# Optimization experiments

Measured on AMD Instinct MI355X. Metric: run time of the kernel, lower is better.

The kernel has to match this reference:

```python
import jax, jax.numpy as jnp
import numpy as np

NC = 20
IMG = 416
SCALES = (13, 26, 52)
B = 64
N = 32


def setup_inputs() -> dict:
    key = jax.random.key(0)
    k1, k2, k3, k4, k5, k6 = jax.random.split(key, 6)
    image = jax.random.normal(k1, (B, 3, IMG, IMG), jnp.float32)
    # Box sizes: multiples of 64 so centers/edges align to all strides (8,16,32);
    # keeps l,r,t,b > 0 inside assigned regions (original code assumes this too).
    wi = jax.random.randint(k2, (B, N), 1, 7)  # w in {64,...,384}
    hi = jax.random.randint(k3, (B, N), 1, 7)
    w = (64 * wi).astype(jnp.float32)
    h = (64 * hi).astype(jnp.float32)
    cx = w / 2 + 32.0 * jax.random.randint(k4, (B, N), 0, (IMG - 64 * wi) // 32 + 1).astype(jnp.float32)
    cy = h / 2 + 32.0 * jax.random.randint(k5, (B, N), 0, (IMG - 64 * hi) // 32 + 1).astype(jnp.float32)
    bboxes = jnp.stack([cx, cy, w, h], axis=-1)  # [B, N, 4] pixel xywh (center format)
    labels = jax.random.randint(k6, (B, N), 0, NC).astype(jnp.int32)
    return {"image": image, "bboxes": bboxes, "labels": labels}


def _assign(boxes, labels, scale):
    """FCOS-style target assignment for one image at one scale. boxes: [N,4], labels: [N]."""
    stride = IMG / scale
    idx = jnp.arange(scale, dtype=jnp.float32)
    centers = (idx + 0.5) * stride  # pixel center of each grid cell

    def step(carry, bl):
        cls, reg = carry
        box, label = bl
        cx, cy, bw, bh = box[0], box[1], box[2], box[3]
        # int() truncation in original == floor for positive values
        pos0, pos1 = jnp.floor(cx / stride), jnp.floor(cy / stride)
        bp0, bp1 = jnp.floor(0.5 * bw / stride), jnp.floor(0.5 * bh / stride)
        ri = (idx >= pos0 - bp0) & (idx < pos0 + bp0)  # i range (dim 0)
        rj = (idx >= pos1 - bp1) & (idx < pos1 + bp1)  # j range (dim 1)
        region = ri[:, None] & rj[None, :]
        hw, hh = jnp.floor(bw / 2), jnp.floor(bh / 2)  # int(boxes[2]/2), int(boxes[3]/2)
        l = centers - (cx - hw)
        r = (cx + hw) - centers
        t = centers - (cy - hh)
        bt = (cy + hh) - centers
        S = scale
        L = jnp.broadcast_to(l[:, None], (S, S))
        R = jnp.broadcast_to(r[:, None], (S, S))
        T = jnp.broadcast_to(t[None, :], (S, S))
        Bo = jnp.broadcast_to(bt[None, :], (S, S))
        m = jnp.maximum(jnp.maximum(L, R), jnp.maximum(T, Bo))
        cent = jnp.sqrt(jnp.minimum(L, R) * jnp.minimum(T, Bo) /
                        (jnp.maximum(L, R) * jnp.maximum(T, Bo)))
        if scale == 13:
            band = m > 256.0
        elif scale == 26:
            band = (m > 64.0) & (m <= 256.0)
        else:
            band = m <= 64.0
        # cls[label, region] = 1
        cls = cls.at[label].set(jnp.where(region, 1.0, cls[label]))
        # sequential min-area-style tie-break: write if untouched or new m < stored max
        regmax = reg.max(axis=0)
        write = region & band & ((regmax == 0.0) | (m < regmax))
        new = jnp.maximum(jnp.stack([L / stride, T / stride, R / stride, Bo / stride, cent]), 0.0)
        reg = jnp.where(write[None], new, reg)
        return (cls, reg), None

    init = (jnp.zeros((NC, scale, scale), jnp.float32),
            jnp.zeros((5, scale, scale), jnp.float32))
    (cls, reg), _ = jax.lax.scan(step, init, (boxes, labels))
    # torch.cat([cls, reg], 0).permute(2, 1, 0) -> [S_j, S_i, 25]
    return jnp.transpose(jnp.concatenate([cls, reg], axis=0), (2, 1, 0))


def reference(image, bboxes, labels):
    targets = [jax.vmap(lambda bx, lb, s=s: _assign(bx, lb, s))(bboxes, labels)
               for s in SCALES]
    return (image, targets[0], targets[1], targets[2])
```

## Files before the change

kernel.cpp:

```cpp
#include <hip/hip_runtime.h>

#define IMG_ELEMS (64 * 3 * 416 * 416)
#define CELLS_PER_IMG (13*13 + 26*26 + 52*52)
#define BASE13 0
#define BASE26 (64 * 169 * 25)
#define BASE52 (BASE26 + 64 * 676 * 25)

__global__ __launch_bounds__(256) void assign_kernel(
    const float* __restrict__ bboxes,
    const int*   __restrict__ labels,
    float* __restrict__ out)
{
    const int b   = blockIdx.x;
    const int tid = threadIdx.x;

    __shared__ float sbox[32][4];
    __shared__ int   slab[32];
    if (tid < 128) ((float*)sbox)[tid] = bboxes[b * 128 + tid];
    if (tid < 32)  slab[tid] = labels[b * 32 + tid];
    __syncthreads();

    int c = blockIdx.y * blockDim.x + tid;
    if (c >= CELLS_PER_IMG) return;

    int S, idx, base, scale_id;
    if (c < 169)      { S = 13; idx = c;       base = BASE13; scale_id = 0; }
    else if (c < 845) { S = 26; idx = c - 169; base = BASE26; scale_id = 1; }
    else              { S = 52; idx = c - 845; base = BASE52; scale_id = 2; }

    const int i = idx % S;
    const int j = idx / S;
    const float stride = 416.0f / (float)S;
    const float inv    = 1.0f / stride;
    const float fi = (float)i, fj = (float)j;
    const float ci = (fi + 0.5f) * stride;
    const float cj = (fj + 0.5f) * stride;

    float reg0 = 0.f, reg1 = 0.f, reg2 = 0.f, reg3 = 0.f, reg4 = 0.f;
    unsigned clsmask = 0u;

    for (int n = 0; n < 32; ++n) {
        const float cx = sbox[n][0], cy = sbox[n][1];
        const float bw = sbox[n][2], bh = sbox[n][3];

        const float pos0 = floorf(cx * inv), pos1 = floorf(cy * inv);
        const float bp0  = floorf(0.5f * bw * inv), bp1 = floorf(0.5f * bh * inv);

        const bool region = (fi >= pos0 - bp0) && (fi < pos0 + bp0) &&
                            (fj >= pos1 - bp1) && (fj < pos1 + bp1);
        if (!region) continue;

        clsmask |= 1u << slab[n];

        const float hw = floorf(0.5f * bw), hh = floorf(0.5f * bh);
        const float L  = ci - (cx - hw);
        const float R  = (cx + hw) - ci;
        const float T  = cj - (cy - hh);
        const float Bo = (cy + hh) - cj;
        const float maxLR = fmaxf(L, R),  minLR = fminf(L, R);
        const float maxTB = fmaxf(T, Bo), minTB = fminf(T, Bo);
        const float m = fmaxf(maxLR, maxTB);

        const bool band = (scale_id == 0) ? (m > 256.0f)
                        : (scale_id == 1) ? (m > 64.0f && m <= 256.0f)
                        :                   (m <= 64.0f);
        if (!band) continue;

        const float regmax = fmaxf(fmaxf(fmaxf(reg0, reg1), fmaxf(reg2, reg3)), reg4);
        if (regmax == 0.0f || m < regmax) {
            const float cent = sqrtf((minLR * minTB) / (maxLR * maxTB));
            reg0 = fmaxf(L  * inv, 0.0f);
            reg1 = fmaxf(T  * inv, 0.0f);
            reg2 = fmaxf(R  * inv, 0.0f);
            reg3 = fmaxf(Bo * inv, 0.0f);
            reg4 = fmaxf(cent,     0.0f);
        }
    }

    float* o = out + base + (((size_t)b * S + j) * S + i) * 25;
    #pragma unroll
    for (int ch = 0; ch < 20; ++ch)
        o[ch] = ((clsmask >> ch) & 1u) ? 1.0f : 0.0f;
    o[20] = reg0; o[21] = reg1; o[22] = reg2; o[23] = reg3; o[24] = reg4;
}

extern "C" void kernel_launch(void* const* d_in, const int* in_sizes, int n_in,
                              void* d_out, int out_size, void* d_ws, size_t ws_size,
                              hipStream_t stream) {
    const float* image  = (const float*)d_in[0];
    const float* bboxes = (const float*)d_in[1];
    const int*   labels = (const int*)  d_in[2];
    float* out = (float*)d_out;

    hipMemcpyAsync(out, image, (size_t)IMG_ELEMS * sizeof(float),
                   hipMemcpyDeviceToDevice, stream);

    dim3 grid(64, (CELLS_PER_IMG + 255) / 256);
    assign_kernel<<<grid, dim3(256), 0, stream>>>(bboxes, labels, out + IMG_ELEMS);
}
```

Measured before the change: 264.3 us.

## Fuse image passthrough copy into assignment kernel with nontemporal vector copies

Replaces the separate hipMemcpyAsync of the image plus the assignment kernel launch with one kernel. The grid is flattened so that the first blocks do target assignment and the remaining blocks copy the image using 16-byte nontemporal loads and stores. This removes one launch and the memcpy-engine path, and lets the copy overlap with the assignment work. The cost is a custom copy whose bandwidth depends on the grid shape and the cache hints.

```diff
diff --git a/kernel.cpp b/kernel.cpp
--- a/kernel.cpp
+++ b/kernel.cpp
@@ -6,13 +6,36 @@
 #define BASE26 (64 * 169 * 25)
 #define BASE52 (BASE26 + 64 * 676 * 25)
 
-__global__ __launch_bounds__(256) void assign_kernel(
+#define ASSIGN_CHUNKS 14
+#define ASSIGN_BLOCKS (64 * ASSIGN_CHUNKS)
+#define N4 (IMG_ELEMS / 4)
+#define COPY_BLOCKS (N4 / 1024)
+
+typedef float v4f __attribute__((ext_vector_type(4)));
+
+__global__ __launch_bounds__(256) void fused_kernel(
+    const v4f* __restrict__ img4,
     const float* __restrict__ bboxes,
     const int*   __restrict__ labels,
     float* __restrict__ out)
 {
-    const int b   = blockIdx.x;
     const int tid = threadIdx.x;
+
+    if (blockIdx.x >= ASSIGN_BLOCKS) {
+        v4f* dst4 = (v4f*)out;
+        const int cb = blockIdx.x - ASSIGN_BLOCKS;
+        const int base = cb * 1024 + tid;
+        #pragma unroll
+        for (int k = 0; k < 4; ++k) {
+            const int idx = base + k * 256;
+            v4f v = __builtin_nontemporal_load(&img4[idx]);
+            __builtin_nontemporal_store(v, &dst4[idx]);
+        }
+        return;
+    }
+
+    const int b     = blockIdx.x / ASSIGN_CHUNKS;
+    const int chunk = blockIdx.x % ASSIGN_CHUNKS;
 
     __shared__ float sbox[32][4];
     __shared__ int   slab[32];
@@ -20,7 +43,7 @@
     if (tid < 32)  slab[tid] = labels[b * 32 + tid];
     __syncthreads();
 
-    int c = blockIdx.y * blockDim.x + tid;
+    const int c = chunk * 256 + tid;
     if (c >= CELLS_PER_IMG) return;
 
     int S, idx, base, scale_id;
@@ -77,7 +100,7 @@
         }
     }
 
-    float* o = out + base + (((size_t)b * S + j) * S + i) * 25;
+    float* o = out + IMG_ELEMS + base + (((size_t)b * S + j) * S + i) * 25;
     #pragma unroll
     for (int ch = 0; ch < 20; ++ch)
         o[ch] = ((clsmask >> ch) & 1u) ? 1.0f : 0.0f;
@@ -92,9 +115,6 @@
     const int*   labels = (const int*)  d_in[2];
     float* out = (float*)d_out;
 
-    hipMemcpyAsync(out, image, (size_t)IMG_ELEMS * sizeof(float),
-                   hipMemcpyDeviceToDevice, stream);
-
-    dim3 grid(64, (CELLS_PER_IMG + 255) / 256);
-    assign_kernel<<<grid, dim3(256), 0, stream>>>(bboxes, labels, out + IMG_ELEMS);
+    fused_kernel<<<dim3(ASSIGN_BLOCKS + COPY_BLOCKS), dim3(256), 0, stream>>>(
+        (const v4f*)image, bboxes, labels, out);
 }
```

After: 249.0 us. -5.8%, faster.
